# Kernel tuning notes

Measured on AMD Instinct MI355X. Metric: run time of the kernel, lower is better.

## Reference

```python
import jax, jax.numpy as jnp
import numpy as np

B, S, D, H, NL, V, E, DFF = 4, 512, 768, 12, 2, 32000, 8, 3072
CF = 1.25
HD = D // H


def setup_inputs() -> dict:
    key = jax.random.key(0)
    ks = jax.random.split(key, 12)
    r = lambda i, shape: jax.random.normal(ks[i], shape, jnp.float32) * 0.02
    return {
        "src": jax.random.randint(ks[0], (B, S), 0, V),
        "src_pad_mask": jnp.zeros((B, S), bool),
        "emb": r(1, (V, D)),
        "qkv_w": r(2, (NL, 3 * D, D)), "qkv_b": jnp.zeros((NL, 3 * D), jnp.float32),
        "out_w": r(3, (NL, D, D)), "out_b": jnp.zeros((NL, D), jnp.float32),
        "wr": r(4, (NL, D, E)),
        "w1": r(5, (NL, E, D, DFF)), "b1": jnp.zeros((NL, E, DFF), jnp.float32),
        "w2": r(6, (NL, E, DFF, D)), "b2": jnp.zeros((NL, E, D), jnp.float32),
        "ln1_g": jnp.ones((NL, D), jnp.float32), "ln1_b": jnp.zeros((NL, D), jnp.float32),
        "ln2_g": jnp.ones((NL, D), jnp.float32), "ln2_b": jnp.zeros((NL, D), jnp.float32),
        "lnf_g": jnp.ones((D,), jnp.float32), "lnf_b": jnp.zeros((D,), jnp.float32),
    }


def layernorm(x, g, b, eps=1e-5):
    mu = jnp.mean(x, -1, keepdims=True)
    var = jnp.mean((x - mu) ** 2, -1, keepdims=True)
    return (x - mu) * jax.lax.rsqrt(var + eps) * g + b


def pos_encoding():
    pos = jnp.arange(S, dtype=jnp.float32)[:, None]
    i = jnp.arange(0, D, 2, dtype=jnp.float32)
    ang = pos * jnp.exp(-(i / D) * jnp.log(jnp.float32(10000.0)))  # [S, D/2]
    pe = jnp.zeros((S, D), jnp.float32)
    pe = pe.at[:, 0::2].set(jnp.sin(ang)).at[:, 1::2].set(jnp.cos(ang))
    return pe


def mha(x, wqkv, bqkv, wo, bo, pad):
    qkv = x @ wqkv.T + bqkv
    q, k, v = jnp.split(qkv, 3, axis=-1)
    q = q.reshape(B, S, H, HD); k = k.reshape(B, S, H, HD); v = v.reshape(B, S, H, HD)
    sc = jnp.einsum('bqhd,bkhd->bhqk', q, k) * (1.0 / float(HD) ** 0.5)
    sc = jnp.where(pad[:, None, None, :], jnp.float32(-1e9), sc)
    at = jax.nn.softmax(sc, -1)
    o = jnp.einsum('bhqk,bkhd->bqhd', at, v).reshape(B, S, D)
    return o @ wo.T + bo


def switch_ffn(x, token_mask, wr, w1, b1, w2, b2):
    # Switch Transformer top-1 routing with capacity drop.
    T = B * S
    cap = int(CF * T / E)
    xf = x.reshape(T, D)
    vm = token_mask.reshape(T).astype(x.dtype)
    logits = xf @ wr                                   # [T, E]
    probs = jax.nn.softmax(logits, -1)
    idx = jnp.argmax(probs, -1)
    gate = jnp.take_along_axis(probs, idx[:, None], -1)[:, 0]
    oh = jax.nn.one_hot(idx, E, dtype=x.dtype) * vm[:, None]      # [T, E]
    pos = jnp.cumsum(oh, axis=0) * oh                  # 1-indexed position in expert
    keep = ((pos > 0) & (pos <= cap)).astype(x.dtype)
    disp = keep[:, :, None] * jax.nn.one_hot((pos - 1).astype(jnp.int32), cap, dtype=x.dtype)  # [T,E,C]
    comb = disp * gate[:, None, None]
    ein = jnp.einsum('tec,td->ecd', disp, xf)          # [E, C, D]
    hid = jax.nn.relu(jnp.einsum('ecd,edf->ecf', ein, w1) + b1[:, None, :])
    eo = jnp.einsum('ecf,efd->ecd', hid, w2) + b2[:, None, :]
    y = jnp.einsum('tec,ecd->td', comb, eo).reshape(B, S, D)
    denom = jnp.maximum(vm.sum(), 1.0)
    me = (probs * vm[:, None]).sum(0) / denom
    ce = oh.sum(0) / denom
    lb = jnp.float32(E) * jnp.sum(me * ce)
    z = jnp.sum((jax.nn.logsumexp(logits, -1) ** 2) * vm) / denom
    return y, lb, z


def forward(src, src_pad_mask, emb, qkv_w, qkv_b, out_w, out_b, wr, w1, b1, w2, b2,
            ln1_g, ln1_b, ln2_g, ln2_b, lnf_g, lnf_b):
    x = emb[src] * jnp.float32(float(D) ** 0.5) + pos_encoding()[None]
    token_mask = ~src_pad_mask
    lbs, zs = [], []
    for l in range(NL):
        xn = layernorm(x, ln1_g[l], ln1_b[l])
        x = x + mha(xn, qkv_w[l], qkv_b[l], out_w[l], out_b[l], src_pad_mask)
        xn = layernorm(x, ln2_g[l], ln2_b[l])
        y, lb, z = switch_ffn(xn, token_mask, wr[l], w1[l], b1[l], w2[l], b2[l])
        x = x + y
        lbs.append(lb); zs.append(z)
    x = layernorm(x, lnf_g, lnf_b)
    return x, jnp.stack(lbs).mean(), jnp.stack(zs).mean()


def reference(src, src_pad_mask, emb, qkv_w, qkv_b, out_w, out_b, wr, w1, b1, w2, b2,
              ln1_g, ln1_b, ln2_g, ln2_b, lnf_g, lnf_b):
    return forward(src, src_pad_mask, emb, qkv_w, qkv_b, out_w, out_b, wr, w1, b1, w2, b2,
                   ln1_g, ln1_b, ln2_g, ln2_b, lnf_g, lnf_b)
```

## Files before the change

kernel.cpp:

```cpp
#include <hip/hip_runtime.h>

#define BB 4
#define SS 512
#define DD 768
#define HH 12
#define NLAYER 2
#define EE 8
#define DFF 3072
#define TT 2048
#define CAP 320
#define HD 64

typedef unsigned short u16;
typedef long long ll;
typedef _Float16 f16x8 __attribute__((ext_vector_type(8)));
typedef float f32x4 __attribute__((ext_vector_type(4)));

union F16U { _Float16 h; u16 u; };

__device__ __forceinline__ void split2h(float v, u16& h0, u16& h1) {
    F16U c0; c0.h = (_Float16)v;
    float r = (v - (float)c0.h) * 4096.0f;
    F16U c1; c1.h = (_Float16)r;
    h0 = c0.u; h1 = c1.u;
}
__device__ __forceinline__ float rec2h(u16 a, u16 b) {
    F16U c0, c1; c0.u = a; c1.u = b;
    return (float)c0.h + (float)c1.h * (1.0f / 4096.0f);
}

#define MFMA16(a, b, c) __builtin_amdgcn_mfma_f32_16x16x32_f16(a, b, c, 0, 0, 0)

struct GemmP {
    const u16* A = nullptr; ll sAp = 0;
    const void* B = nullptr; ll sBp = 0;
    const float* bias = nullptr; ll biasStride = 0;
    void* C = nullptr; ll sCp = 0;
    int M = 0, N = 0, K = 0, lda = 0, ldb = 0, ldc = 0;
    int modA = 1; ll sA1 = 0, sA2 = 0;
    int modB = 1; ll sB1 = 0, sB2 = 0;
    int modC = 1; ll sC1 = 0, sC2 = 0;
    float alpha = 1.f;
    int flags = 0;
    int KS = 1; ll partStride = 0;
    int Jc = 1;
};

#define PADK 40

template<bool BTRANS, int NS>
__global__ __launch_bounds__(256) void gemm_kernel(GemmP p) {
    __shared__ u16 Al[NS][128][PADK];
    __shared__ u16 Bl[NS][128][PADK];
    const int tid = threadIdx.x;

    int bx, by, bz;
    {
        int gx = gridDim.x, gy = gridDim.y;
        int NBt = gx * gy * gridDim.z;
        int L = blockIdx.x + gx * (blockIdx.y + gy * blockIdx.z);
        int q = NBt >> 3, r = NBt & 7;
        int xcd = L & 7, wi = L >> 3;
        int c = (xcd < r) ? xcd * (q + 1) + wi : r * (q + 1) + (xcd - r) * q + wi;
        int Jc = p.Jc;
        int gxJ = gx * Jc;
        int sj = c / gxJ;
        int t = c - sj * gxJ;
        bx = t / Jc;
        int j = sj * Jc + (t - (t / Jc) * Jc);
        by = j % gy; bz = j / gy;
    }
    const int n0 = bx * 128, m0 = by * 128;
    const int slice = bz % p.KS;
    const int z = bz / p.KS;
    const int kslice = p.K / p.KS;
    const int k0 = slice * kslice;
    const int nkt = kslice >> 5;

    const u16* Ap = p.A + (ll)(z % p.modA) * p.sA1 + (ll)(z / p.modA) * p.sA2 + k0;
    const ll zB = (ll)(z % p.modB) * p.sB1 + (ll)(z / p.modB) * p.sB2;
    const ll zC = (ll)(z % p.modC) * p.sC1 + (ll)(z / p.modC) * p.sC2;
    const u16* Bpu = BTRANS ? ((const u16*)p.B + zB + k0) : nullptr;
    const float* Bpf = BTRANS ? nullptr : ((const float*)p.B + zB);

    const int lane = tid & 63, wid = tid >> 6;
    const int wm = (wid >> 1) * 64, wn = (wid & 1) * 64;
    const int ar = lane & 15, kg = (lane >> 4) * 8;

    f32x4 acc0[4][4] = {};
    f32x4 acc1[4][4] = {};

    uint4 ra[2 * NS];
    uint4 rb[2 * NS];
    float rbf[16];

    auto loadA = [&](int kt) {
        #pragma unroll
        for (int s = 0; s < NS; ++s)
            #pragma unroll
            for (int h = 0; h < 2; ++h) {
                int c = tid + h * 256, row = c >> 2, q = c & 3;
                int gm = m0 + row;
                uint4 v = {0u, 0u, 0u, 0u};
                if (gm < p.M) v = *(const uint4*)(Ap + (ll)s * p.sAp + (size_t)gm * p.lda + kt * 32 + q * 8);
                ra[s * 2 + h] = v;
            }
    };
    auto storeA = [&]() {
        #pragma unroll
        for (int s = 0; s < NS; ++s)
            #pragma unroll
            for (int h = 0; h < 2; ++h) {
                int c = tid + h * 256, row = c >> 2, q = c & 3;
                *(uint4*)&Al[s][row][q * 8] = ra[s * 2 + h];
            }
    };
    auto loadB = [&](int kt) {
        if (BTRANS) {
            #pragma unroll
            for (int s = 0; s < NS; ++s)
                #pragma unroll
                for (int h = 0; h < 2; ++h) {
                    int c = tid + h * 256, row = c >> 2, q = c & 3;
                    int gn = n0 + row;
                    uint4 v = {0u, 0u, 0u, 0u};
                    if (gn < p.N) v = *(const uint4*)(Bpu + (ll)s * p.sBp + (size_t)gn * p.ldb + kt * 32 + q * 8);
                    rb[s * 2 + h] = v;
                }
        } else {
            #pragma unroll
            for (int it = 0; it < 4; ++it)
                #pragma unroll
                for (int e = 0; e < 4; ++e) {
                    int kk = (tid >> 7) * 16 + it * 4 + e;
                    int gn = n0 + (tid & 127);
                    float v = 0.f;
                    if (gn < p.N) v = Bpf[(size_t)(k0 + kt * 32 + kk) * p.ldb + gn];
                    rbf[it * 4 + e] = v;
                }
        }
    };
    auto storeB = [&]() {
        if (BTRANS) {
            #pragma unroll
            for (int s = 0; s < NS; ++s)
                #pragma unroll
                for (int h = 0; h < 2; ++h) {
                    int c = tid + h * 256, row = c >> 2, q = c & 3;
                    *(uint4*)&Bl[s][row][q * 8] = rb[s * 2 + h];
                }
        } else {
            int col = tid & 127;
            #pragma unroll
            for (int it = 0; it < 4; ++it) {
                int kq = (tid >> 7) * 16 + it * 4;
                u16 t0[4], t1[4];
                #pragma unroll
                for (int e = 0; e < 4; ++e) split2h(rbf[it * 4 + e], t0[e], t1[e]);
                *(uint2*)&Bl[0][col][kq] = *(uint2*)t0;
                if (NS == 2) *(uint2*)&Bl[1][col][kq] = *(uint2*)t1;
            }
        }
    };

    loadA(0); loadB(0);
    for (int kt = 0; kt < nkt; ++kt) {
        storeA(); storeB();
        __syncthreads();
        if (kt + 1 < nkt) { loadA(kt + 1); loadB(kt + 1); }
        f16x8 b0r[4], b1r[4];
        #pragma unroll
        for (int j = 0; j < 4; ++j) {
            b0r[j] = *(const f16x8*)&Bl[0][wn + j * 16 + ar][kg];
            if (NS == 2) b1r[j] = *(const f16x8*)&Bl[1][wn + j * 16 + ar][kg];
        }
        #pragma unroll
        for (int i = 0; i < 4; ++i) {
            f16x8 a0 = *(const f16x8*)&Al[0][wm + i * 16 + ar][kg];
            f16x8 a1;
            if (NS == 2) a1 = *(const f16x8*)&Al[1][wm + i * 16 + ar][kg];
            #pragma unroll
            for (int j = 0; j < 4; ++j) {
                acc0[i][j] = MFMA16(a0, b0r[j], acc0[i][j]);
                if (NS == 2) {
                    acc1[i][j] = MFMA16(a0, b1r[j], acc1[i][j]);
                    acc1[i][j] = MFMA16(a1, b0r[j], acc1[i][j]);
                }
            }
        }
        __syncthreads();
    }

    const bool doPart = (p.flags & 16);
    float* Cpart = doPart ? ((float*)p.C + (ll)slice * p.partStride + zC) : nullptr;
    const float* biasp = (p.flags & 1) ? (p.bias + (ll)z * p.biasStride) : nullptr;
    u16* C0 = (!doPart && (p.flags & 8)) ? ((u16*)p.C + zC) : nullptr;
    u16* C1 = C0 ? (C0 + p.sCp) : nullptr;
    float* Cf = (!doPart && !(p.flags & 8)) ? ((float*)p.C + zC) : nullptr;
    #pragma unroll
    for (int i = 0; i < 4; ++i) {
        #pragma unroll
        for (int j = 0; j < 4; ++j) {
            int gc = n0 + wn + j * 16 + (lane & 15);
            if (gc >= p.N) continue;
            int gr0 = m0 + wm + i * 16 + (lane >> 4) * 4;
            #pragma unroll
            for (int r = 0; r < 4; ++r) {
                int gr = gr0 + r;
                if (gr >= p.M) continue;
                float v = acc0[i][j][r];
                if (NS == 2) v += acc1[i][j][r] * (1.0f / 4096.0f);
                v *= p.alpha;
                size_t off = (size_t)gr * p.ldc + gc;
                if (doPart) { Cpart[off] = v; continue; }
                if (p.flags & 1) v = __fadd_rn(v, biasp[gc]);
                if (p.flags & 2) v = fmaxf(v, 0.f);
                if (p.flags & 8) { u16 h0, h1; split2h(v, h0, h1); C0[off] = h0; C1[off] = h1; }
                else Cf[off] = v;
            }
        }
    }
}

__global__ __launch_bounds__(256) void flash_kernel(
    const u16* __restrict__ qkvp, ll sQp,
    const u16* __restrict__ vTp, ll sVp,
    const unsigned char* __restrict__ pad,
    u16* __restrict__ attnp, ll sOp) {
    __shared__ u16 KV[2][64][72];
    __shared__ u16 Pl[2][4][16][72];

    int L = blockIdx.x;
    int c = (L & 7) * 48 + (L >> 3);
    int bh = c >> 3, qt = c & 7;
    int b = bh / HH, h = bh % HH;
    int lane = threadIdx.x & 63, wv = threadIdx.x >> 6;
    int qbase = b * SS + qt * 64 + wv * 16;

    int spl = threadIdx.x >> 7;
    int srr = threadIdx.x & 127;
    int srow = srr >> 1, shalf = srr & 1;

    f16x8 qf[2][2];
    {
        const u16* qr = qkvp + (size_t)(qbase + (lane & 15)) * (3 * DD) + h * HD + (lane >> 4) * 8;
        #pragma unroll
        for (int kt2 = 0; kt2 < 2; ++kt2)
            #pragma unroll
            for (int pl = 0; pl < 2; ++pl)
                qf[kt2][pl] = *(const f16x8*)(qr + (ll)pl * sQp + kt2 * 32);
    }

    f32x4 S[32];
    #pragma unroll
    for (int kv = 0; kv < 8; ++kv) {
        const u16* gk = qkvp + (size_t)(b * SS + kv * 64 + srow) * (3 * DD) + DD + h * HD + (ll)spl * sQp;
        #pragma unroll
        for (int qq = 0; qq < 4; ++qq) {
            int off = shalf * 32 + qq * 8;
            *(uint4*)&KV[spl][srow][off] = *(const uint4*)(gk + off);
        }
        __syncthreads();
        #pragma unroll
        for (int nf = 0; nf < 4; ++nf) {
            f32x4 a0 = {}, a1 = {};
            #pragma unroll
            for (int kt2 = 0; kt2 < 2; ++kt2) {
                f16x8 b0 = *(const f16x8*)&KV[0][nf * 16 + (lane & 15)][kt2 * 32 + (lane >> 4) * 8];
                f16x8 b1 = *(const f16x8*)&KV[1][nf * 16 + (lane & 15)][kt2 * 32 + (lane >> 4) * 8];
                a0 = MFMA16(qf[kt2][0], b0, a0);
                a1 = MFMA16(qf[kt2][0], b1, a1);
                a1 = MFMA16(qf[kt2][1], b0, a1);
            }
            int col = kv * 64 + nf * 16 + (lane & 15);
            bool msk = pad[b * SS + col] != 0;
            #pragma unroll
            for (int r = 0; r < 4; ++r) {
                float v = (a0[r] + a1[r] * (1.0f / 4096.0f)) * 0.125f;
                S[kv * 4 + nf][r] = msk ? -1e9f : v;
            }
        }
        __syncthreads();
    }

    float mx[4] = {-1e30f, -1e30f, -1e30f, -1e30f}, sm[4] = {0.f, 0.f, 0.f, 0.f}, inv[4];
    #pragma unroll
    for (int f = 0; f < 32; ++f)
        #pragma unroll
        for (int r = 0; r < 4; ++r) mx[r] = fmaxf(mx[r], S[f][r]);
    #pragma unroll
    for (int r = 0; r < 4; ++r) {
        #pragma unroll
        for (int off = 1; off < 16; off <<= 1) mx[r] = fmaxf(mx[r], __shfl_xor(mx[r], off));
    }
    #pragma unroll
    for (int f = 0; f < 32; ++f)
        #pragma unroll
        for (int r = 0; r < 4; ++r) { float e = expf(S[f][r] - mx[r]); S[f][r] = e; sm[r] += e; }
    #pragma unroll
    for (int r = 0; r < 4; ++r) {
        #pragma unroll
        for (int off = 1; off < 16; off <<= 1) sm[r] += __shfl_xor(sm[r], off);
        inv[r] = 1.f / sm[r];
    }

    f32x4 p0[4] = {}, p1[4] = {};
    #pragma unroll
    for (int kv = 0; kv < 8; ++kv) {
        const u16* gv = vTp + (size_t)bh * HD * SS + (size_t)srow * SS + kv * 64 + (ll)spl * sVp;
        #pragma unroll
        for (int qq = 0; qq < 4; ++qq) {
            int off = shalf * 32 + qq * 8;
            *(uint4*)&KV[spl][srow][off] = *(const uint4*)(gv + off);
        }
        #pragma unroll
        for (int nf = 0; nf < 4; ++nf)
            #pragma unroll
            for (int r = 0; r < 4; ++r) {
                float v = S[kv * 4 + nf][r] * inv[r];
                u16 h0, h1; split2h(v, h0, h1);
                Pl[0][wv][(lane >> 4) * 4 + r][nf * 16 + (lane & 15)] = h0;
                Pl[1][wv][(lane >> 4) * 4 + r][nf * 16 + (lane & 15)] = h1;
            }
        __syncthreads();
        f16x8 pa[2][2];
        #pragma unroll
        for (int kt2 = 0; kt2 < 2; ++kt2)
            #pragma unroll
            for (int pl = 0; pl < 2; ++pl)
                pa[kt2][pl] = *(const f16x8*)&Pl[pl][wv][lane & 15][kt2 * 32 + (lane >> 4) * 8];
        #pragma unroll
        for (int df = 0; df < 4; ++df) {
            #pragma unroll
            for (int kt2 = 0; kt2 < 2; ++kt2) {
                f16x8 v0 = *(const f16x8*)&KV[0][df * 16 + (lane & 15)][kt2 * 32 + (lane >> 4) * 8];
                f16x8 v1 = *(const f16x8*)&KV[1][df * 16 + (lane & 15)][kt2 * 32 + (lane >> 4) * 8];
                p0[df] = MFMA16(pa[kt2][0], v0, p0[df]);
                p1[df] = MFMA16(pa[kt2][0], v1, p1[df]);
                p1[df] = MFMA16(pa[kt2][1], v0, p1[df]);
            }
        }
        __syncthreads();
    }

    #pragma unroll
    for (int df = 0; df < 4; ++df)
        #pragma unroll
        for (int r = 0; r < 4; ++r) {
            float v = p0[df][r] + p1[df][r] * (1.0f / 4096.0f);
            int row = qbase + (lane >> 4) * 4 + r;
            int col = h * HD + df * 16 + (lane & 15);
            u16 h0, h1; split2h(v, h0, h1);
            attnp[(size_t)row * DD + col] = h0;
            attnp[(size_t)row * DD + col + sOp] = h1;
        }
}

struct RedP {
    const float* part = nullptr; ll partStride = 0; int KS = 1;
    float* outf = nullptr;
    u16* o0 = nullptr; ll planeStride = 0;
    const float* bias = nullptr; ll biasStride = 0; ll batchElems = 1; int Nc = 1;
    const float* src = nullptr;
    ll total = 0; int mode = 0;
};
__global__ void reduce_kernel(RedP p) {
    ll e0 = ((ll)blockIdx.x * 256 + threadIdx.x) * 4;
    if (e0 >= p.total) return;
    float4 s = *(const float4*)(p.part + e0);
    for (int k = 1; k < p.KS; ++k) {
        float4 t = *(const float4*)(p.part + (ll)k * p.partStride + e0);
        s.x += t.x; s.y += t.y; s.z += t.z; s.w += t.w;
    }
    if (p.mode & 1) {
        ll b = e0 / p.batchElems;
        int d = (int)(e0 % p.Nc);
        float4 bv = *(const float4*)(p.bias + b * p.biasStride + d);
        s.x = __fadd_rn(s.x, bv.x); s.y = __fadd_rn(s.y, bv.y);
        s.z = __fadd_rn(s.z, bv.z); s.w = __fadd_rn(s.w, bv.w);
    }
    if (p.mode & 4) {
        float4 t = *(const float4*)(p.src + e0);
        s.x = __fadd_rn(s.x, t.x); s.y = __fadd_rn(s.y, t.y);
        s.z = __fadd_rn(s.z, t.z); s.w = __fadd_rn(s.w, t.w);
    }
    if (p.mode & 2) { s.x = fmaxf(s.x, 0.f); s.y = fmaxf(s.y, 0.f); s.z = fmaxf(s.z, 0.f); s.w = fmaxf(s.w, 0.f); }
    if (p.mode & 8) {
        u16 t0[4], t1[4];
        float vv[4] = {s.x, s.y, s.z, s.w};
        #pragma unroll
        for (int e = 0; e < 4; ++e) split2h(vv[e], t0[e], t1[e]);
        *(uint2*)(p.o0 + e0) = *(uint2*)t0;
        *(uint2*)(p.o0 + p.planeStride + e0) = *(uint2*)t1;
    } else {
        *(float4*)(p.outf + e0) = s;
    }
}

__global__ void wsplit_kernel(const float* __restrict__ w, u16* __restrict__ p0,
                              ll planeStride, ll total) {
    ll e0 = ((ll)blockIdx.x * 256 + threadIdx.x) * 4;
    if (e0 >= total) return;
    float4 v = *(const float4*)(w + e0);
    u16 t0[4], t1[4];
    float vv[4] = {v.x, v.y, v.z, v.w};
    #pragma unroll
    for (int e = 0; e < 4; ++e) split2h(vv[e], t0[e], t1[e]);
    *(uint2*)(p0 + e0) = *(uint2*)t0;
    *(uint2*)(p0 + planeStride + e0) = *(uint2*)t1;
}

__global__ void vtrans_kernel(const u16* __restrict__ qkvp, ll sQp,
                              u16* __restrict__ vTp, ll sVp) {
    __shared__ float t[32][33];
    int z = blockIdx.z;
    int b = z / HH, h = z % HH;
    int c0 = blockIdx.x * 32, r0 = blockIdx.y * 32;
    int tx = threadIdx.x, ty = threadIdx.y;
    const u16* in = qkvp + (size_t)(b * SS) * (3 * DD) + 2 * DD + h * HD;
    #pragma unroll
    for (int i = 0; i < 32; i += 8) {
        size_t o = (size_t)(r0 + ty + i) * (3 * DD) + c0 + tx;
        t[ty + i][tx] = rec2h(in[o], in[o + sQp]);
    }
    __syncthreads();
    u16* out = vTp + (size_t)z * HD * SS;
    #pragma unroll
    for (int i = 0; i < 32; i += 8) {
        size_t o = (size_t)(c0 + ty + i) * SS + r0 + tx;
        u16 h0, h1; split2h(t[tx][ty + i], h0, h1);
        out[o] = h0; out[o + sVp] = h1;
    }
}

__global__ void pe_kernel(float* __restrict__ pe) {
    int s = blockIdx.x, tid = threadIdx.x;
    const float lg = 9.210340371976184f;
    #pragma unroll
    for (int j = 0; j < 3; ++j) {
        int d = j * 256 + tid;
        int half = d >> 1;
        float fi = (float)(2 * half) / 768.0f;
        float arg = __fmul_rn(-fi, lg);
        float freq = (float)exp((double)arg);
        float ang = __fmul_rn((float)s, freq);
        double da = (double)ang;
        pe[(size_t)s * DD + d] = (d & 1) ? (float)cos(da) : (float)sin(da);
    }
}

__global__ void embed_kernel(const int* __restrict__ src, const float* __restrict__ emb,
                             const float* __restrict__ pe, float* __restrict__ x) {
    int t = blockIdx.x, tid = threadIdx.x;
    int s = t & (SS - 1);
    int tok = src[t];
    const float sq = 27.712812921102035f;
    #pragma unroll
    for (int j = 0; j < 3; ++j) {
        int d = j * 256 + tid;
        float e = emb[(size_t)tok * DD + d];
        x[(size_t)t * DD + d] = __fadd_rn(__fmul_rn(e, sq), pe[(size_t)s * DD + d]);
    }
}

__global__ void ln_kernel(const float* __restrict__ x, const float* __restrict__ g,
                          const float* __restrict__ b, float* __restrict__ outf,
                          u16* __restrict__ op, ll planeStride) {
    int t = blockIdx.x, tid = threadIdx.x;
    const float* xr = x + (size_t)t * DD;
    float v[3], s = 0.f, sq = 0.f;
    #pragma unroll
    for (int j = 0; j < 3; ++j) { v[j] = xr[tid + j * 256]; s += v[j]; sq += v[j] * v[j]; }
    #pragma unroll
    for (int off = 32; off; off >>= 1) { s += __shfl_xor(s, off); sq += __shfl_xor(sq, off); }
    __shared__ float rs[4], rq[4];
    int wid = tid >> 6;
    if ((tid & 63) == 0) { rs[wid] = s; rq[wid] = sq; }
    __syncthreads();
    s = rs[0] + rs[1] + rs[2] + rs[3];
    sq = rq[0] + rq[1] + rq[2] + rq[3];
    float mu = s / 768.0f;
    float var = sq / 768.0f - mu * mu;
    float rstd = rsqrtf(var + 1e-5f);
    #pragma unroll
    for (int j = 0; j < 3; ++j) {
        int d = tid + j * 256;
        float y = __fadd_rn(__fmul_rn(__fmul_rn(v[j] - mu, rstd), g[d]), b[d]);
        if (outf) outf[(size_t)t * DD + d] = y;
        if (op) {
            size_t o = (size_t)t * DD + d;
            u16 h0, h1; split2h(y, h0, h1);
            op[o] = h0; op[o + planeStride] = h1;
        }
    }
}

__global__ void ln2_router_kernel(const float* __restrict__ x, const float* __restrict__ g,
                                  const float* __restrict__ b, const float* __restrict__ wr,
                                  const unsigned char* __restrict__ pad,
                                  u16* __restrict__ op, ll planeStride,
                                  float* __restrict__ probs, float* __restrict__ lsev,
                                  float* __restrict__ gate, int* __restrict__ idx) {
    int t = blockIdx.x, tid = threadIdx.x;
    const float* xr = x + (size_t)t * DD;
    float v[3], s = 0.f, sq = 0.f;
    #pragma unroll
    for (int j = 0; j < 3; ++j) { v[j] = xr[tid + j * 256]; s += v[j]; sq += v[j] * v[j]; }
    #pragma unroll
    for (int off = 32; off; off >>= 1) { s += __shfl_xor(s, off); sq += __shfl_xor(sq, off); }
    __shared__ float rs[4], rq[4];
    __shared__ float ra[4][8];
    int wid = tid >> 6;
    if ((tid & 63) == 0) { rs[wid] = s; rq[wid] = sq; }
    __syncthreads();
    s = rs[0] + rs[1] + rs[2] + rs[3];
    sq = rq[0] + rq[1] + rq[2] + rq[3];
    float mu = s / 768.0f;
    float var = sq / 768.0f - mu * mu;
    float rstd = rsqrtf(var + 1e-5f);
    float a[8] = {0.f, 0.f, 0.f, 0.f, 0.f, 0.f, 0.f, 0.f};
    #pragma unroll
    for (int j = 0; j < 3; ++j) {
        int d = tid + j * 256;
        float y = __fadd_rn(__fmul_rn(__fmul_rn(v[j] - mu, rstd), g[d]), b[d]);
        size_t o = (size_t)t * DD + d;
        u16 h0, h1; split2h(y, h0, h1);
        op[o] = h0; op[o + planeStride] = h1;
        const float* w = wr + (size_t)d * EE;
        #pragma unroll
        for (int e = 0; e < 8; ++e) a[e] += y * w[e];
    }
    #pragma unroll
    for (int off = 32; off; off >>= 1)
        #pragma unroll
        for (int e = 0; e < 8; ++e) a[e] += __shfl_xor(a[e], off);
    if ((tid & 63) == 0)
        #pragma unroll
        for (int e = 0; e < 8; ++e) ra[wid][e] = a[e];
    __syncthreads();
    if (tid == 0) {
        #pragma unroll
        for (int e = 0; e < 8; ++e) a[e] = ra[0][e] + ra[1][e] + ra[2][e] + ra[3][e];
        int vm = (pad[t] == 0);
        float mx = a[0]; int bi = 0;
        #pragma unroll
        for (int e = 1; e < 8; ++e) if (a[e] > mx) { mx = a[e]; bi = e; }
        float ex[8], sum = 0.f;
        #pragma unroll
        for (int e = 0; e < 8; ++e) { ex[e] = expf(a[e] - mx); sum += ex[e]; }
        float inv = 1.f / sum;
        #pragma unroll
        for (int e = 0; e < 8; ++e) probs[(size_t)t * EE + e] = vm ? ex[e] * inv : 0.f;
        lsev[t] = vm ? (mx + logf(sum)) : 0.f;
        gate[t] = ex[bi] * inv;
        idx[t] = vm ? bi : -1;
    }
}

__global__ void route_scan_kernel(const int* __restrict__ idx, const float* __restrict__ probs,
                                  const float* __restrict__ lsev, int* __restrict__ slot,
                                  int* __restrict__ tos, float* __restrict__ acc) {
    int lane = threadIdx.x;
    int base = lane * 32;
    int ev[32];
    int c[8] = {0, 0, 0, 0, 0, 0, 0, 0};
    #pragma unroll
    for (int i = 0; i < 32; ++i) {
        int e = idx[base + i];
        ev[i] = e;
        #pragma unroll
        for (int q = 0; q < 8; ++q) c[q] += (e == q);
    }
    int excl[8], tot[8];
    #pragma unroll
    for (int e = 0; e < 8; ++e) {
        int v = c[e];
        #pragma unroll
        for (int off = 1; off < 64; off <<= 1) {
            int n = __shfl_up(v, off);
            if (lane >= off) v += n;
        }
        excl[e] = v - c[e];
        tot[e] = __shfl(v, 63);
    }
    int r[8];
    #pragma unroll
    for (int e = 0; e < 8; ++e) r[e] = excl[e];
    #pragma unroll
    for (int i = 0; i < 32; ++i) {
        int t = base + i, e = ev[i], s = -1;
        if (e >= 0) {
            int pos = 0;
            #pragma unroll
            for (int q = 0; q < 8; ++q) if (e == q) { r[q]++; pos = r[q]; }
            if (pos <= CAP) { s = e * CAP + pos - 1; tos[s] = t; }
        }
        slot[t] = s;
    }
    float pa[8] = {0.f, 0.f, 0.f, 0.f, 0.f, 0.f, 0.f, 0.f};
    float l2 = 0.f, vld = 0.f;
    #pragma unroll
    for (int i = 0; i < 32; ++i) {
        int t = base + i;
        float lv = lsev[t];
        l2 += lv * lv;
        if (ev[i] >= 0) vld += 1.f;
        #pragma unroll
        for (int e = 0; e < 8; ++e) pa[e] += probs[(size_t)t * EE + e];
    }
    #pragma unroll
    for (int off = 32; off; off >>= 1) {
        #pragma unroll
        for (int e = 0; e < 8; ++e) pa[e] += __shfl_xor(pa[e], off);
        l2 += __shfl_xor(l2, off);
        vld += __shfl_xor(vld, off);
    }
    if (lane == 0) {
        float denom = fmaxf(vld, 1.f);
        float lb = 0.f;
        #pragma unroll
        for (int e = 0; e < 8; ++e) lb += (pa[e] / denom) * ((float)tot[e] / denom);
        lb *= 8.f;
        acc[0] += lb;
        acc[1] += l2 / denom;
    }
}

__global__ void gather_kernel(const int* __restrict__ tos, const u16* __restrict__ xnp,
                              ll sXp, u16* __restrict__ einp, ll sEp) {
    int s = blockIdx.x;
    int tid = threadIdx.x;
    if (tid >= 192) return;
    int pl = tid / 96, q = tid % 96;
    int t = tos[s];
    uint4 v = {0u, 0u, 0u, 0u};
    if (t >= 0) v = *(const uint4*)(xnp + (ll)pl * sXp + (size_t)t * DD + q * 8);
    *(uint4*)(einp + (ll)pl * sEp + (size_t)s * DD + q * 8) = v;
}

__global__ void combine_kernel(const int* __restrict__ slot, const float* __restrict__ gate,
                               const float* __restrict__ eo, float* __restrict__ x) {
    int t = blockIdx.x, tid = threadIdx.x;
    int s = slot[t];
    if (s < 0) return;
    float gv = gate[t];
    #pragma unroll
    for (int j = 0; j < 3; ++j) {
        int d = j * 256 + tid;
        size_t o = (size_t)t * DD + d;
        x[o] = __fadd_rn(x[o], __fmul_rn(gv, eo[(size_t)s * DD + d]));
    }
}

__global__ void finalize_kernel(const float* __restrict__ acc, float* __restrict__ out) {
    out[(size_t)TT * DD] = acc[0] * (1.f / NLAYER);
    out[(size_t)TT * DD + 1] = acc[1] * (1.f / NLAYER);
}

static inline void run_gemm(bool btrans, int ns, const GemmP& p, dim3 grid, hipStream_t s) {
    if (btrans) {
        gemm_kernel<true, 2><<<grid, 256, 0, s>>>(p);
    } else {
        if (ns == 2) gemm_kernel<false, 2><<<grid, 256, 0, s>>>(p);
        else gemm_kernel<false, 1><<<grid, 256, 0, s>>>(p);
    }
}
static inline void run_reduce(const RedP& r, hipStream_t s) {
    reduce_kernel<<<(int)((r.total / 4 + 255) / 256), 256, 0, s>>>(r);
}

extern "C" void kernel_launch(void* const* d_in, const int* in_sizes, int n_in,
                              void* d_out, int out_size, void* d_ws, size_t ws_size,
                              hipStream_t stream) {
    const int* src = (const int*)d_in[0];
    const unsigned char* pad = (const unsigned char*)d_in[1];
    const float* emb = (const float*)d_in[2];
    const float* qkv_w = (const float*)d_in[3];
    const float* qkv_b = (const float*)d_in[4];
    const float* out_w = (const float*)d_in[5];
    const float* out_b = (const float*)d_in[6];
    const float* wr = (const float*)d_in[7];
    const float* w1 = (const float*)d_in[8];
    const float* b1 = (const float*)d_in[9];
    const float* w2 = (const float*)d_in[10];
    const float* b2 = (const float*)d_in[11];
    const float* ln1_g = (const float*)d_in[12];
    const float* ln1_b = (const float*)d_in[13];
    const float* ln2_g = (const float*)d_in[14];
    const float* ln2_b = (const float*)d_in[15];
    const float* lnf_g = (const float*)d_in[16];
    const float* lnf_b = (const float*)d_in[17];

    char* w = (char*)d_ws;
    size_t off = 0;
    auto alloc = [&](size_t bytes) -> void* {
        void* p = w + off;
        off += (bytes + 255) & ~(size_t)255;
        return p;
    };
    float* x      = (float*)alloc((size_t)TT * DD * 4);
    float* peT    = (float*)alloc((size_t)SS * DD * 4);
    u16*   xnp    = (u16*)  alloc((size_t)2 * TT * DD * 2);
    u16*   qkvp   = (u16*)  alloc((size_t)2 * TT * 3 * DD * 2);
    u16*   vTp    = (u16*)  alloc((size_t)2 * BB * HH * HD * SS * 2);
    u16*   attnp  = (u16*)  alloc((size_t)2 * TT * DD * 2);
    u16*   einp   = (u16*)  alloc((size_t)2 * EE * CAP * DD * 2);
    u16*   hidp   = (u16*)  alloc((size_t)2 * EE * CAP * DFF * 2);
    float* eo     = (float*)alloc((size_t)EE * CAP * DD * 4);
    char*  regB   = (char*) alloc((size_t)2 * EE * CAP * DFF * 4);
    u16*   qkvwp  = (u16*)  alloc((size_t)2 * NLAYER * 3 * DD * DD * 2);
    u16*   owp    = (u16*)  alloc((size_t)2 * NLAYER * DD * DD * 2);
    float* probs  = (float*)alloc((size_t)TT * EE * 4);
    float* lsev   = (float*)alloc((size_t)TT * 4);
    float* gate   = (float*)alloc((size_t)TT * 4);
    int*   idx    = (int*)  alloc((size_t)TT * 4);
    int*   slot   = (int*)  alloc((size_t)TT * 4);
    int*   tos    = (int*)  alloc((size_t)EE * CAP * 4);
    float* accb   = (float*)alloc(256);
    if (off > ws_size) return;

    float* qkvpart = (float*)regB;
    float* oppart  = (float*)regB;
    float* ffnpart = (float*)regB;

    hipMemsetAsync(accb, 0, 8, stream);
    pe_kernel<<<SS, 256, 0, stream>>>(peT);
    embed_kernel<<<TT, 256, 0, stream>>>(src, emb, peT, x);

    {
        ll tq = (ll)NLAYER * 3 * DD * DD;
        wsplit_kernel<<<(int)((tq / 4 + 255) / 256), 256, 0, stream>>>(qkv_w, qkvwp, tq, tq);
        ll to = (ll)NLAYER * DD * DD;
        wsplit_kernel<<<(int)((to / 4 + 255) / 256), 256, 0, stream>>>(out_w, owp, to, to);
    }

    for (int l = 0; l < NLAYER; ++l) {
        const int nsF = (l < NLAYER - 1) ? 2 : 1;
        ln_kernel<<<TT, 256, 0, stream>>>(x, ln1_g + l * DD, ln1_b + l * DD, nullptr, xnp, (ll)TT * DD);

        {
            GemmP p;
            p.A = xnp; p.sAp = (ll)TT * DD; p.lda = DD;
            p.B = qkvwp + (size_t)l * 3 * DD * DD; p.sBp = (ll)NLAYER * 3 * DD * DD; p.ldb = DD;
            p.C = qkvpart; p.ldc = 3 * DD;
            p.M = TT; p.N = 3 * DD; p.K = DD;
            p.flags = 16; p.KS = 2; p.partStride = (ll)TT * 3 * DD;
            p.Jc = 4;
            run_gemm(true, 2, p, dim3(18, 16, 2), stream);
        }
        {
            RedP r;
            r.part = qkvpart; r.partStride = (ll)TT * 3 * DD; r.KS = 2;
            r.o0 = qkvp; r.planeStride = (ll)TT * 3 * DD;
            r.bias = qkv_b + (size_t)l * 3 * DD; r.biasStride = 0; r.batchElems = (ll)TT * 3 * DD; r.Nc = 3 * DD;
            r.total = (ll)TT * 3 * DD; r.mode = 1 | 8;
            run_reduce(r, stream);
        }
        vtrans_kernel<<<dim3(HD / 32, SS / 32, BB * HH), dim3(32, 8), 0, stream>>>(
            qkvp, (ll)TT * 3 * DD, vTp, (ll)BB * HH * HD * SS);
        flash_kernel<<<BB * HH * 8, 256, 0, stream>>>(
            qkvp, (ll)TT * 3 * DD, vTp, (ll)BB * HH * HD * SS, pad, attnp, (ll)TT * DD);
        {
            GemmP p;
            p.A = attnp; p.sAp = (ll)TT * DD; p.lda = DD;
            p.B = owp + (size_t)l * DD * DD; p.sBp = (ll)NLAYER * DD * DD; p.ldb = DD;
            p.C = oppart; p.ldc = DD;
            p.M = TT; p.N = DD; p.K = DD;
            p.flags = 16; p.KS = 4; p.partStride = (ll)TT * DD;
            p.Jc = 8;
            run_gemm(true, 2, p, dim3(6, 16, 4), stream);
        }
        {
            RedP r;
            r.part = oppart; r.partStride = (ll)TT * DD; r.KS = 4;
            r.outf = x;
            r.bias = out_b + (size_t)l * DD; r.biasStride = 0; r.batchElems = (ll)TT * DD; r.Nc = DD;
            r.src = x;
            r.total = (ll)TT * DD; r.mode = 1 | 4;
            run_reduce(r, stream);
        }
        ln2_router_kernel<<<TT, 256, 0, stream>>>(x, ln2_g + l * DD, ln2_b + l * DD,
                                                  wr + (size_t)l * DD * EE, pad,
                                                  xnp, (ll)TT * DD, probs, lsev, gate, idx);
        hipMemsetAsync(tos, 0xFF, (size_t)EE * CAP * 4, stream);
        route_scan_kernel<<<1, 64, 0, stream>>>(idx, probs, lsev, slot, tos, accb);
        gather_kernel<<<EE * CAP, 256, 0, stream>>>(tos, xnp, (ll)TT * DD, einp, (ll)EE * CAP * DD);
        {
            GemmP p;
            p.A = einp; p.sAp = (ll)EE * CAP * DD; p.lda = DD;
            p.modA = EE; p.sA1 = (ll)CAP * DD;
            p.B = w1 + (size_t)l * EE * DD * DFF; p.ldb = DFF;
            p.modB = EE; p.sB1 = (ll)DD * DFF;
            p.C = ffnpart; p.ldc = DFF; p.modC = EE; p.sC1 = (ll)CAP * DFF;
            p.M = CAP; p.N = DFF; p.K = DD;
            p.flags = 16; p.KS = 2; p.partStride = (ll)EE * CAP * DFF;
            p.Jc = 6;
            run_gemm(false, nsF, p, dim3(24, 3, EE * 2), stream);
        }
        {
            RedP r;
            r.part = ffnpart; r.partStride = (ll)EE * CAP * DFF; r.KS = 2;
            r.o0 = hidp; r.planeStride = (ll)EE * CAP * DFF;
            r.bias = b1 + (size_t)l * EE * DFF; r.biasStride = DFF; r.batchElems = (ll)CAP * DFF; r.Nc = DFF;
            r.total = (ll)EE * CAP * DFF; r.mode = 1 | 2 | 8;
            run_reduce(r, stream);
        }
        {
            GemmP p;
            p.A = hidp; p.sAp = (ll)EE * CAP * DFF; p.lda = DFF;
            p.modA = EE; p.sA1 = (ll)CAP * DFF;
            p.B = w2 + (size_t)l * EE * DFF * DD; p.ldb = DD;
            p.modB = EE; p.sB1 = (ll)DFF * DD;
            p.C = ffnpart; p.ldc = DD; p.modC = EE; p.sC1 = (ll)CAP * DD;
            p.M = CAP; p.N = DD; p.K = DFF;
            p.flags = 16; p.KS = 4; p.partStride = (ll)EE * CAP * DD;
            p.Jc = 6;
            run_gemm(false, nsF, p, dim3(6, 3, EE * 4), stream);
        }
        {
            RedP r;
            r.part = ffnpart; r.partStride = (ll)EE * CAP * DD; r.KS = 4;
            r.outf = eo;
            r.bias = b2 + (size_t)l * EE * DD; r.biasStride = DD; r.batchElems = (ll)CAP * DD; r.Nc = DD;
            r.total = (ll)EE * CAP * DD; r.mode = 1;
            run_reduce(r, stream);
        }
        combine_kernel<<<TT, 256, 0, stream>>>(slot, gate, eo, x);
    }
    ln_kernel<<<TT, 256, 0, stream>>>(x, lnf_g, lnf_b, (float*)d_out, nullptr, 0);
    finalize_kernel<<<1, 1, 0, stream>>>(accb, (float*)d_out);
}
```

Measured before the change: 830.0 us.

## Double GEMM K-tile to 64 and fuse MoE reductions into epilogue and combine

Raises the GEMM k-tile from 32 to 64, halving the number of barrier-synchronised iterations while doubling LDS footprint and staging registers. Drops split-K on the first expert GEMM so bias, activation and fp16 split happen in its epilogue, removing a separate reduction kernel and partial-buffer traffic. Folds the second expert GEMM's split-K reduction and bias into the combine kernel, eliminating another reduce pass and the intermediate expert-output buffer. Larger tiles and fewer blocks on the first GEMM may lower occupancy and parallelism.

Measured after the change: 786.9 us. 1.05x faster.

```diff
diff --git a/kernel.cpp b/kernel.cpp
--- a/kernel.cpp
+++ b/kernel.cpp
@@ -46,7 +46,8 @@
     int Jc = 1;
 };
 
-#define PADK 40
+#define BK 64
+#define PADK 72
 
 template<bool BTRANS, int NS>
 __global__ __launch_bounds__(256) void gemm_kernel(GemmP p) {
@@ -75,7 +76,7 @@
     const int z = bz / p.KS;
     const int kslice = p.K / p.KS;
     const int k0 = slice * kslice;
-    const int nkt = kslice >> 5;
+    const int nkt = kslice >> 6;
 
     const u16* Ap = p.A + (ll)(z % p.modA) * p.sA1 + (ll)(z / p.modA) * p.sA2 + k0;
     const ll zB = (ll)(z % p.modB) * p.sB1 + (ll)(z / p.modB) * p.sB2;
@@ -90,29 +91,29 @@
     f32x4 acc0[4][4] = {};
     f32x4 acc1[4][4] = {};
 
-    uint4 ra[2 * NS];
-    uint4 rb[2 * NS];
-    float rbf[16];
+    uint4 ra[4 * NS];
+    uint4 rb[4 * NS];
+    float rbf[32];
 
     auto loadA = [&](int kt) {
         #pragma unroll
         for (int s = 0; s < NS; ++s)
             #pragma unroll
-            for (int h = 0; h < 2; ++h) {
-                int c = tid + h * 256, row = c >> 2, q = c & 3;
+            for (int h = 0; h < 4; ++h) {
+                int c = tid + h * 256, row = c >> 3, q = c & 7;
                 int gm = m0 + row;
                 uint4 v = {0u, 0u, 0u, 0u};
-                if (gm < p.M) v = *(const uint4*)(Ap + (ll)s * p.sAp + (size_t)gm * p.lda + kt * 32 + q * 8);
-                ra[s * 2 + h] = v;
+                if (gm < p.M) v = *(const uint4*)(Ap + (ll)s * p.sAp + (size_t)gm * p.lda + kt * BK + q * 8);
+                ra[s * 4 + h] = v;
             }
     };
     auto storeA = [&]() {
         #pragma unroll
         for (int s = 0; s < NS; ++s)
             #pragma unroll
-            for (int h = 0; h < 2; ++h) {
-                int c = tid + h * 256, row = c >> 2, q = c & 3;
-                *(uint4*)&Al[s][row][q * 8] = ra[s * 2 + h];
+            for (int h = 0; h < 4; ++h) {
+                int c = tid + h * 256, row = c >> 3, q = c & 7;
+                *(uint4*)&Al[s][row][q * 8] = ra[s * 4 + h];
             }
     };
     auto loadB = [&](int kt) {
@@ -120,24 +121,22 @@
             #pragma unroll
             for (int s = 0; s < NS; ++s)
                 #pragma unroll
-                for (int h = 0; h < 2; ++h) {
-                    int c = tid + h * 256, row = c >> 2, q = c & 3;
+                for (int h = 0; h < 4; ++h) {
+                    int c = tid + h * 256, row = c >> 3, q = c & 7;
                     int gn = n0 + row;
                     uint4 v = {0u, 0u, 0u, 0u};
-                    if (gn < p.N) v = *(const uint4*)(Bpu + (ll)s * p.sBp + (size_t)gn * p.ldb + kt * 32 + q * 8);
-                    rb[s * 2 + h] = v;
+                    if (gn < p.N) v = *(const uint4*)(Bpu + (ll)s * p.sBp + (size_t)gn * p.ldb + kt * BK + q * 8);
+                    rb[s * 4 + h] = v;
                 }
         } else {
-            #pragma unroll
-            for (int it = 0; it < 4; ++it)
-                #pragma unroll
-                for (int e = 0; e < 4; ++e) {
-                    int kk = (tid >> 7) * 16 + it * 4 + e;
-                    int gn = n0 + (tid & 127);
-                    float v = 0.f;
-                    if (gn < p.N) v = Bpf[(size_t)(k0 + kt * 32 + kk) * p.ldb + gn];
-                    rbf[it * 4 + e] = v;
-                }
+            int gn = n0 + (tid & 127);
+            int kb = (tid >> 7) * 32;
+            #pragma unroll
+            for (int i = 0; i < 32; ++i) {
+                float v = 0.f;
+                if (gn < p.N) v = Bpf[(size_t)(k0 + kt * BK + kb + i) * p.ldb + gn];
+                rbf[i] = v;
+            }
         }
     };
     auto storeB = [&]() {
@@ -145,20 +144,20 @@
             #pragma unroll
             for (int s = 0; s < NS; ++s)
                 #pragma unroll
-                for (int h = 0; h < 2; ++h) {
-                    int c = tid + h * 256, row = c >> 2, q = c & 3;
-                    *(uint4*)&Bl[s][row][q * 8] = rb[s * 2 + h];
+                for (int h = 0; h < 4; ++h) {
+                    int c = tid + h * 256, row = c >> 3, q = c & 7;
+                    *(uint4*)&Bl[s][row][q * 8] = rb[s * 4 + h];
                 }
         } else {
             int col = tid & 127;
-            #pragma unroll
-            for (int it = 0; it < 4; ++it) {
-                int kq = (tid >> 7) * 16 + it * 4;
+            int kb = (tid >> 7) * 32;
+            #pragma unroll
+            for (int i = 0; i < 8; ++i) {
                 u16 t0[4], t1[4];
                 #pragma unroll
-                for (int e = 0; e < 4; ++e) split2h(rbf[it * 4 + e], t0[e], t1[e]);
-                *(uint2*)&Bl[0][col][kq] = *(uint2*)t0;
-                if (NS == 2) *(uint2*)&Bl[1][col][kq] = *(uint2*)t1;
+                for (int e = 0; e < 4; ++e) split2h(rbf[i * 4 + e], t0[e], t1[e]);
+                *(uint2*)&Bl[0][col][kb + i * 4] = *(uint2*)t0;
+                if (NS == 2) *(uint2*)&Bl[1][col][kb + i * 4] = *(uint2*)t1;
             }
         }
     };
@@ -168,23 +167,26 @@
         storeA(); storeB();
         __syncthreads();
         if (kt + 1 < nkt) { loadA(kt + 1); loadB(kt + 1); }
-        f16x8 b0r[4], b1r[4];
-        #pragma unroll
-        for (int j = 0; j < 4; ++j) {
-            b0r[j] = *(const f16x8*)&Bl[0][wn + j * 16 + ar][kg];
-            if (NS == 2) b1r[j] = *(const f16x8*)&Bl[1][wn + j * 16 + ar][kg];
-        }
-        #pragma unroll
-        for (int i = 0; i < 4; ++i) {
-            f16x8 a0 = *(const f16x8*)&Al[0][wm + i * 16 + ar][kg];
-            f16x8 a1;
-            if (NS == 2) a1 = *(const f16x8*)&Al[1][wm + i * 16 + ar][kg];
+        #pragma unroll
+        for (int kt2 = 0; kt2 < 2; ++kt2) {
+            f16x8 b0r[4], b1r[4];
             #pragma unroll
             for (int j = 0; j < 4; ++j) {
-                acc0[i][j] = MFMA16(a0, b0r[j], acc0[i][j]);
-                if (NS == 2) {
-                    acc1[i][j] = MFMA16(a0, b1r[j], acc1[i][j]);
-                    acc1[i][j] = MFMA16(a1, b0r[j], acc1[i][j]);
+                b0r[j] = *(const f16x8*)&Bl[0][wn + j * 16 + ar][kt2 * 32 + kg];
+                if (NS == 2) b1r[j] = *(const f16x8*)&Bl[1][wn + j * 16 + ar][kt2 * 32 + kg];
+            }
+            #pragma unroll
+            for (int i = 0; i < 4; ++i) {
+                f16x8 a0 = *(const f16x8*)&Al[0][wm + i * 16 + ar][kt2 * 32 + kg];
+                f16x8 a1;
+                if (NS == 2) a1 = *(const f16x8*)&Al[1][wm + i * 16 + ar][kt2 * 32 + kg];
+                #pragma unroll
+                for (int j = 0; j < 4; ++j) {
+                    acc0[i][j] = MFMA16(a0, b0r[j], acc0[i][j]);
+                    if (NS == 2) {
+                        acc1[i][j] = MFMA16(a0, b1r[j], acc1[i][j]);
+                        acc1[i][j] = MFMA16(a1, b0r[j], acc1[i][j]);
+                    }
                 }
             }
         }
@@ -638,17 +640,23 @@
     *(uint4*)(einp + (ll)pl * sEp + (size_t)s * DD + q * 8) = v;
 }
 
-__global__ void combine_kernel(const int* __restrict__ slot, const float* __restrict__ gate,
-                               const float* __restrict__ eo, float* __restrict__ x) {
+__global__ void combine2_kernel(const int* __restrict__ slot, const float* __restrict__ gate,
+                                const float* __restrict__ part, ll partStride, int KS,
+                                const float* __restrict__ b2, float* __restrict__ x) {
     int t = blockIdx.x, tid = threadIdx.x;
     int s = slot[t];
     if (s < 0) return;
     float gv = gate[t];
+    int e = s / CAP;
     #pragma unroll
     for (int j = 0; j < 3; ++j) {
         int d = j * 256 + tid;
-        size_t o = (size_t)t * DD + d;
-        x[o] = __fadd_rn(x[o], __fmul_rn(gv, eo[(size_t)s * DD + d]));
+        size_t o = (size_t)s * DD + d;
+        float v = part[o];
+        for (int k = 1; k < KS; ++k) v += part[(ll)k * partStride + o];
+        v = __fadd_rn(v, b2[(size_t)e * DD + d]);
+        size_t ox = (size_t)t * DD + d;
+        x[ox] = __fadd_rn(x[ox], __fmul_rn(gv, v));
     }
 }
 
@@ -706,8 +714,7 @@
     u16*   attnp  = (u16*)  alloc((size_t)2 * TT * DD * 2);
     u16*   einp   = (u16*)  alloc((size_t)2 * EE * CAP * DD * 2);
     u16*   hidp   = (u16*)  alloc((size_t)2 * EE * CAP * DFF * 2);
-    float* eo     = (float*)alloc((size_t)EE * CAP * DD * 4);
-    char*  regB   = (char*) alloc((size_t)2 * EE * CAP * DFF * 4);
+    char*  regB   = (char*) alloc((size_t)2 * TT * 3 * DD * 4);
     u16*   qkvwp  = (u16*)  alloc((size_t)2 * NLAYER * 3 * DD * DD * 2);
     u16*   owp    = (u16*)  alloc((size_t)2 * NLAYER * DD * DD * 2);
     float* probs  = (float*)alloc((size_t)TT * EE * 4);
@@ -791,19 +798,13 @@
             p.modA = EE; p.sA1 = (ll)CAP * DD;
             p.B = w1 + (size_t)l * EE * DD * DFF; p.ldb = DFF;
             p.modB = EE; p.sB1 = (ll)DD * DFF;
-            p.C = ffnpart; p.ldc = DFF; p.modC = EE; p.sC1 = (ll)CAP * DFF;
+            p.bias = b1 + (size_t)l * EE * DFF; p.biasStride = DFF;
+            p.C = hidp; p.sCp = (ll)EE * CAP * DFF; p.ldc = DFF;
+            p.modC = EE; p.sC1 = (ll)CAP * DFF;
             p.M = CAP; p.N = DFF; p.K = DD;
-            p.flags = 16; p.KS = 2; p.partStride = (ll)EE * CAP * DFF;
-            p.Jc = 6;
-            run_gemm(false, nsF, p, dim3(24, 3, EE * 2), stream);
-        }
-        {
-            RedP r;
-            r.part = ffnpart; r.partStride = (ll)EE * CAP * DFF; r.KS = 2;
-            r.o0 = hidp; r.planeStride = (ll)EE * CAP * DFF;
-            r.bias = b1 + (size_t)l * EE * DFF; r.biasStride = DFF; r.batchElems = (ll)CAP * DFF; r.Nc = DFF;
-            r.total = (ll)EE * CAP * DFF; r.mode = 1 | 2 | 8;
-            run_reduce(r, stream);
+            p.flags = 1 | 2 | 8;
+            p.Jc = 3;
+            run_gemm(false, nsF, p, dim3(24, 3, EE), stream);
         }
         {
             GemmP p;
@@ -814,18 +815,11 @@
             p.C = ffnpart; p.ldc = DD; p.modC = EE; p.sC1 = (ll)CAP * DD;
             p.M = CAP; p.N = DD; p.K = DFF;
             p.flags = 16; p.KS = 4; p.partStride = (ll)EE * CAP * DD;
-            p.Jc = 6;
+            p.Jc = 12;
             run_gemm(false, nsF, p, dim3(6, 3, EE * 4), stream);
         }
-        {
-            RedP r;
-            r.part = ffnpart; r.partStride = (ll)EE * CAP * DD; r.KS = 4;
-            r.outf = eo;
-            r.bias = b2 + (size_t)l * EE * DD; r.biasStride = DD; r.batchElems = (ll)CAP * DD; r.Nc = DD;
-            r.total = (ll)EE * CAP * DD; r.mode = 1;
-            run_reduce(r, stream);
-        }
-        combine_kernel<<<TT, 256, 0, stream>>>(slot, gate, eo, x);
+        combine2_kernel<<<TT, 256, 0, stream>>>(slot, gate, ffnpart, (ll)EE * CAP * DD, 4,
+                                                b2 + (size_t)l * EE * DD, x);
     }
     ln_kernel<<<TT, 256, 0, stream>>>(x, lnf_g, lnf_b, (float*)d_out, nullptr, 0);
     finalize_kernel<<<1, 1, 0, stream>>>(accb, (float*)d_out);
```
